# Optimization experiments

Measured on AMD Instinct MI355X. Metric: run time of the kernel, lower is better.

## Reference

```python
import jax, jax.numpy as jnp
import numpy as np

NUM_BINS = 64
R = 2                      # kernel_radius = ceil(2*sigma), sigma=1
NB = NUM_BINS + 2 * R      # 68 padded bins
EPS = 1e-8


def _bspline(d):
    # cubic B-spline Parzen kernel, sigma=1 so d/sigma == d
    ad = jnp.abs(d)
    return jnp.where(
        ad < 1.0, (3.0 * ad ** 3 - 6.0 * ad ** 2 + 4.0) / 6.0,
        jnp.where(ad < 2.0, (2.0 - ad) ** 3 / 6.0, jnp.zeros_like(ad)))


def setup_inputs() -> dict:
    key = jax.random.key(0)
    k1, k2 = jax.random.split(key)
    shape = (2, 1, 80, 80, 80)
    source = jax.random.normal(k1, shape, dtype=jnp.float32)
    target = jax.random.normal(k2, shape, dtype=jnp.float32)
    return {"source": source, "target": target}


def _win(x):
    # x: [B, N] flattened voxels (mask=None, sample_rate=1 keeps all voxels)
    # returns win_idx [B, 2R, N] int32 and bspline weights [B, 2R, N]
    mx = jax.lax.stop_gradient(jnp.max(x, axis=1))            # [B]
    mn = jax.lax.stop_gradient(jnp.min(x, axis=1))            # [B]
    bw = (mx - mn) / NUM_BINS                                 # bin width
    pad_min = mn - bw * R
    pos = (x - pad_min[:, None]) / bw[:, None]                # [B, N]
    idx = jax.lax.stop_gradient(
        jnp.clip(jnp.floor(pos), R, R + NUM_BINS - 1))        # detached floor+clamp
    min_win = (idx - R + 1).astype(jnp.int32)                 # [B, N]
    r = jnp.arange(2 * R, dtype=jnp.int32)                    # [2R]
    win_idx = min_win[:, None, :] + r[None, :, None]          # [B, 2R, N]
    # bin_center is arange(NB), so gathered centers == win_idx as float
    w = _bspline(pos[:, None, :] - win_idx.astype(x.dtype))   # [B, 2R, N]
    return win_idx, w


def _densify(win_idx, w):
    # scatter-add window weights into dense [B, NB, N] bin-weight matrix.
    # (Equivalent to the torch eq-mask-and-sum loop: window indices are distinct.)
    B, _, N = w.shape
    col = jnp.broadcast_to(jnp.arange(N), win_idx.shape[1:])  # [2R, N]
    def per_b(ib, wb):
        return jnp.zeros((NB, N), wb.dtype).at[ib, col].add(wb)
    return jax.vmap(per_b)(win_idx, w)


def reference(source, target):
    B = source.shape[0]
    s = source.reshape(B, -1)   # [B, N]
    t = target.reshape(B, -1)
    si, sw = _win(s)
    ti, tw = _win(t)
    sbw = _densify(si, sw)      # [B, NB, N]
    tbw = _densify(ti, tw)      # [B, NB, N]
    source_hist = sbw.sum(-1)   # [B, NB]
    target_hist = tbw.sum(-1)
    joint_hist = jnp.einsum('bin,bjn->bij', sbw, tbw)   # [B, NB, NB]
    source_density = source_hist / jnp.maximum(source_hist.sum(-1, keepdims=True), EPS)
    target_density = target_hist / jnp.maximum(target_hist.sum(-1, keepdims=True), EPS)
    joint_density = joint_hist / jnp.maximum(joint_hist.sum(axis=(1, 2), keepdims=True), EPS)
    return (source_density, target_density, joint_density)
```

## Files before the change

kernel.cpp:

```cpp
#include <hip/hip_runtime.h>
#include <float.h>

#define NB 68
#define NJ (NB * NB)
#define NSLICE 4
#define HTPB 1024
#define MMBLK 125
#define SCALE 8192.0f


__global__ __launch_bounds__(1024) void k_prep(const float* __restrict__ src,
                                               const float* __restrict__ tgt,
                                               float4* __restrict__ P,
                                               unsigned* __restrict__ J,
                                               int n4) {
    __shared__ float red[16][4];
    const int b = blockIdx.y;
    const int lin = (b * gridDim.x + blockIdx.x) * 1024 + threadIdx.x;
    if (lin < NSLICE * 2 * NJ) J[lin] = 0u;

    const int i = blockIdx.x * 1024 + threadIdx.x;
    float smx = -FLT_MAX, smn = FLT_MAX, tmx = -FLT_MAX, tmn = FLT_MAX;
    if (i < n4) {
        float4 v = ((const float4*)src)[(size_t)b * n4 + i];
        float4 w = ((const float4*)tgt)[(size_t)b * n4 + i];
        smx = fmaxf(fmaxf(v.x, v.y), fmaxf(v.z, v.w));
        smn = fminf(fminf(v.x, v.y), fminf(v.z, v.w));
        tmx = fmaxf(fmaxf(w.x, w.y), fmaxf(w.z, w.w));
        tmn = fminf(fminf(w.x, w.y), fminf(w.z, w.w));
    }
#pragma unroll
    for (int m = 1; m < 64; m <<= 1) {
        smx = fmaxf(smx, __shfl_xor(smx, m));
        smn = fminf(smn, __shfl_xor(smn, m));
        tmx = fmaxf(tmx, __shfl_xor(tmx, m));
        tmn = fminf(tmn, __shfl_xor(tmn, m));
    }
    const int wave = threadIdx.x >> 6;
    if ((threadIdx.x & 63) == 0) {
        red[wave][0] = smx;
        red[wave][1] = smn;
        red[wave][2] = tmx;
        red[wave][3] = tmn;
    }
    __syncthreads();
    if (threadIdx.x == 0) {
#pragma unroll
        for (int k = 1; k < 16; ++k) {
            smx = fmaxf(smx, red[k][0]);
            smn = fminf(smn, red[k][1]);
            tmx = fmaxf(tmx, red[k][2]);
            tmn = fminf(tmn, red[k][3]);
        }
        P[b * 128 + blockIdx.x] = make_float4(smx, smn, tmx, tmn);
    }
}

__device__ __forceinline__ float bspl(float d) {
    float ad = fabsf(d);
    float a = (3.0f * ad * ad * ad - 6.0f * ad * ad + 4.0f) * (1.0f / 6.0f);
    float t = 2.0f - ad;
    float c = t * t * t * (1.0f / 6.0f);
    return ad < 1.0f ? a : (ad < 2.0f ? c : 0.0f);
}

__device__ __forceinline__ void vox1(float sv, float tv, unsigned* jh,
                                     float spad, float sinv, float tpad,
                                     float tinv) {
    float posS = (sv - spad) * sinv;
    float fS = floorf(posS);
    fS = fminf(fmaxf(fS, 2.0f), 65.0f);
    int si = (int)fS - 1;
    float dS = posS - fS;
    float a[4] = {bspl(dS + 1.0f), bspl(dS), bspl(dS - 1.0f), bspl(dS - 2.0f)};

    float posT = (tv - tpad) * tinv;
    float fT = floorf(posT);
    fT = fminf(fmaxf(fT, 2.0f), 65.0f);
    int ti = (int)fT - 1;
    float dT = posT - fT;
    float bb[4] = {bspl(dT + 1.0f), bspl(dT), bspl(dT - 1.0f), bspl(dT - 2.0f)};

    unsigned* base = jh + si * NB + ti;
#pragma unroll
    for (int r = 0; r < 4; ++r) {
#pragma unroll
        for (int c = 0; c < 4; ++c) {
            unsigned q = (unsigned)(a[r] * bb[c] * SCALE + 0.5f);
            atomicAdd(&base[r * NB + c], q);
        }
    }
}

__global__ __launch_bounds__(HTPB) void k_hist(
    const float* __restrict__ src, const float* __restrict__ tgt,
    const float4* __restrict__ P, unsigned* __restrict__ J, int n4) {
    __shared__ unsigned lh[2 * NJ];
    __shared__ float pmm[8], mmv[4];
    const int tid = threadIdx.x;
    const int b = blockIdx.y;

    if (tid < 128) {
        float smx = -FLT_MAX, smn = FLT_MAX, tmx = -FLT_MAX, tmn = FLT_MAX;
        if (tid < MMBLK) {
            float4 v = P[b * 128 + tid];
            smx = v.x; smn = v.y; tmx = v.z; tmn = v.w;
        }
#pragma unroll
        for (int m = 1; m < 64; m <<= 1) {
            smx = fmaxf(smx, __shfl_xor(smx, m));
            smn = fminf(smn, __shfl_xor(smn, m));
            tmx = fmaxf(tmx, __shfl_xor(tmx, m));
            tmn = fminf(tmn, __shfl_xor(tmn, m));
        }
        if ((tid & 63) == 0) {
            int w = tid >> 6;
            pmm[w * 4 + 0] = smx;
            pmm[w * 4 + 1] = smn;
            pmm[w * 4 + 2] = tmx;
            pmm[w * 4 + 3] = tmn;
        }
    }
    uint4* z4 = (uint4*)lh;
    const uint4 zz = make_uint4(0u, 0u, 0u, 0u);
    for (int i = tid; i < (2 * NJ) / 4; i += HTPB) z4[i] = zz;
    __syncthreads();
    if (tid == 0) {
        mmv[0] = fmaxf(pmm[0], pmm[4]);
        mmv[1] = fminf(pmm[1], pmm[5]);
        mmv[2] = fmaxf(pmm[2], pmm[6]);
        mmv[3] = fminf(pmm[3], pmm[7]);
    }
    __syncthreads();

    const float sbw = (mmv[0] - mmv[1]) * (1.0f / 64.0f);
    const float tbw = (mmv[2] - mmv[3]) * (1.0f / 64.0f);
    const float sinv = 1.0f / sbw, tinv = 1.0f / tbw;
    const float spad = mmv[1] - 2.0f * sbw;
    const float tpad = mmv[3] - 2.0f * tbw;

    unsigned* jh = lh + (tid & 1) * NJ;
    const int i0 = blockIdx.x * HTPB + tid;
    if (i0 < n4) {
        float4 sA = ((const float4*)src)[(size_t)b * n4 + i0];
        float4 tA = ((const float4*)tgt)[(size_t)b * n4 + i0];
        vox1(sA.x, tA.x, jh, spad, sinv, tpad, tinv);
        vox1(sA.y, tA.y, jh, spad, sinv, tpad, tinv);
        vox1(sA.z, tA.z, jh, spad, sinv, tpad, tinv);
        vox1(sA.w, tA.w, jh, spad, sinv, tpad, tinv);
    }
    __syncthreads();

    const int rot = (blockIdx.x * 1327) % NJ;
    unsigned* Jb = J + ((size_t)(blockIdx.x & (NSLICE - 1)) * 2 + b) * NJ;
    for (int k = tid; k < NJ; k += HTPB) {
        int i = k + rot;
        if (i >= NJ) i -= NJ;
        unsigned s = lh[i] + lh[NJ + i];
        if (s) atomicAdd(&Jb[i], s);
    }
}

__global__ __launch_bounds__(1024) void k_norm(
    const unsigned* __restrict__ J, float* __restrict__ out, double inv) {
    __shared__ float jf[NJ];
    __shared__ float part[NB][8];
    const int b = blockIdx.x;
    const int tid = threadIdx.x;

    for (int i = tid; i < NJ; i += 1024) {
        unsigned s = 0u;
#pragma unroll
        for (int sl = 0; sl < NSLICE; ++sl)
            s += J[((size_t)sl * 2 + b) * NJ + i];
        float f = (float)((double)s * inv);
        jf[i] = f;
        out[4 * NB + b * NJ + i] = f;
    }
    __syncthreads();

    if (tid < 8 * NB) {
        int r = tid >> 3, k = tid & 7;
        float s = 0.0f;
#pragma unroll
        for (int j = 0; j < 9; ++j) {
            int c = k + 8 * j;
            if (c < NB) s += jf[r * NB + c];
        }
        part[r][k] = s;
    }
    __syncthreads();
    if (tid < NB) {
        float s = part[tid][0] + part[tid][1] + part[tid][2] + part[tid][3] +
                  part[tid][4] + part[tid][5] + part[tid][6] + part[tid][7];
        out[b * NB + tid] = s;
    }
    __syncthreads();

    if (tid < 8 * NB) {
        int c = tid >> 3, k = tid & 7;
        float s = 0.0f;
#pragma unroll
        for (int j = 0; j < 9; ++j) {
            int r = k + 8 * j;
            if (r < NB) s += jf[r * NB + c];
        }
        part[c][k] = s;
    }
    __syncthreads();
    if (tid < NB) {
        float s = part[tid][0] + part[tid][1] + part[tid][2] + part[tid][3] +
                  part[tid][4] + part[tid][5] + part[tid][6] + part[tid][7];
        out[2 * NB + b * NB + tid] = s;
    }
}

extern "C" void kernel_launch(void* const* d_in, const int* in_sizes, int n_in,
                              void* d_out, int out_size, void* d_ws,
                              size_t ws_size, hipStream_t stream) {
    const float* src = (const float*)d_in[0];
    const float* tgt = (const float*)d_in[1];
    float* out = (float*)d_out;
    float4* P = (float4*)((char*)d_ws + 64);
    unsigned* J = (unsigned*)((char*)d_ws + 4160);
    const int nvox = in_sizes[0] / 2;
    const int n4 = nvox / 4;
    const double inv = 1.0 / ((double)nvox * (double)SCALE);

    k_prep<<<dim3(MMBLK, 2), dim3(1024), 0, stream>>>(src, tgt, P, J, n4);
    k_hist<<<dim3(MMBLK, 2), dim3(HTPB), 0, stream>>>(src, tgt, P, J, n4);
    k_norm<<<dim3(2), dim3(1024), 0, stream>>>(J, out, inv);
}
```

Before: 22.15 us.

## Pack histogram atomics into 64-bit pairs with parity-offset LDS copies

Each voxel's 16 shared-memory 32-bit atomic adds become 8 64-bit atomic adds, with two adjacent bin counts packed into one 64-bit word. To keep the 64-bit targets 8-byte aligned, the two LDS histogram copies are now chosen by the parity of the target bin, the second copy offset by one word, instead of by thread parity. The quantization scale doubles to SCALE 16384. This relies on no carry crossing between the packed 32-bit halves, which holds only while per-block counts stay under 2^32. Larger counts at the doubled scale bring that limit closer.

```diff
diff --git a/kernel.cpp b/kernel.cpp
--- a/kernel.cpp
+++ b/kernel.cpp
@@ -6,7 +6,8 @@
 #define NSLICE 4
 #define HTPB 1024
 #define MMBLK 125
-#define SCALE 8192.0f
+#define SCALE 16384.0f
+#define LHSZ (2 * NJ + 8)
 
 
 __global__ __launch_bounds__(1024) void k_prep(const float* __restrict__ src,
@@ -64,7 +65,7 @@
     return ad < 1.0f ? a : (ad < 2.0f ? c : 0.0f);
 }
 
-__device__ __forceinline__ void vox1(float sv, float tv, unsigned* jh,
+__device__ __forceinline__ void vox1(float sv, float tv, unsigned* lh,
                                      float spad, float sinv, float tpad,
                                      float tinv) {
     float posS = (sv - spad) * sinv;
@@ -79,23 +80,27 @@
     fT = fminf(fmaxf(fT, 2.0f), 65.0f);
     int ti = (int)fT - 1;
     float dT = posT - fT;
-    float bb[4] = {bspl(dT + 1.0f), bspl(dT), bspl(dT - 1.0f), bspl(dT - 2.0f)};
-
-    unsigned* base = jh + si * NB + ti;
+    float b0 = bspl(dT + 1.0f), b1 = bspl(dT), b2 = bspl(dT - 1.0f),
+          b3 = bspl(dT - 2.0f);
+
+    unsigned* base = lh + ((ti & 1) ? (NJ + 1) : 0) + si * NB + ti;
 #pragma unroll
     for (int r = 0; r < 4; ++r) {
-#pragma unroll
-        for (int c = 0; c < 4; ++c) {
-            unsigned q = (unsigned)(a[r] * bb[c] * SCALE + 0.5f);
-            atomicAdd(&base[r * NB + c], q);
-        }
+        unsigned q0 = (unsigned)(a[r] * b0 * SCALE + 0.5f);
+        unsigned q1 = (unsigned)(a[r] * b1 * SCALE + 0.5f);
+        unsigned q2 = (unsigned)(a[r] * b2 * SCALE + 0.5f);
+        unsigned q3 = (unsigned)(a[r] * b3 * SCALE + 0.5f);
+        atomicAdd((unsigned long long*)(base + r * NB),
+                  (unsigned long long)q0 | ((unsigned long long)q1 << 32));
+        atomicAdd((unsigned long long*)(base + r * NB + 2),
+                  (unsigned long long)q2 | ((unsigned long long)q3 << 32));
     }
 }
 
 __global__ __launch_bounds__(HTPB) void k_hist(
     const float* __restrict__ src, const float* __restrict__ tgt,
     const float4* __restrict__ P, unsigned* __restrict__ J, int n4) {
-    __shared__ unsigned lh[2 * NJ];
+    __shared__ __align__(16) unsigned lh[LHSZ];
     __shared__ float pmm[8], mmv[4];
     const int tid = threadIdx.x;
     const int b = blockIdx.y;
@@ -123,7 +128,7 @@
     }
     uint4* z4 = (uint4*)lh;
     const uint4 zz = make_uint4(0u, 0u, 0u, 0u);
-    for (int i = tid; i < (2 * NJ) / 4; i += HTPB) z4[i] = zz;
+    for (int i = tid; i < LHSZ / 4; i += HTPB) z4[i] = zz;
     __syncthreads();
     if (tid == 0) {
         mmv[0] = fmaxf(pmm[0], pmm[4]);
@@ -139,15 +144,14 @@
     const float spad = mmv[1] - 2.0f * sbw;
     const float tpad = mmv[3] - 2.0f * tbw;
 
-    unsigned* jh = lh + (tid & 1) * NJ;
     const int i0 = blockIdx.x * HTPB + tid;
     if (i0 < n4) {
         float4 sA = ((const float4*)src)[(size_t)b * n4 + i0];
         float4 tA = ((const float4*)tgt)[(size_t)b * n4 + i0];
-        vox1(sA.x, tA.x, jh, spad, sinv, tpad, tinv);
-        vox1(sA.y, tA.y, jh, spad, sinv, tpad, tinv);
-        vox1(sA.z, tA.z, jh, spad, sinv, tpad, tinv);
-        vox1(sA.w, tA.w, jh, spad, sinv, tpad, tinv);
+        vox1(sA.x, tA.x, lh, spad, sinv, tpad, tinv);
+        vox1(sA.y, tA.y, lh, spad, sinv, tpad, tinv);
+        vox1(sA.z, tA.z, lh, spad, sinv, tpad, tinv);
+        vox1(sA.w, tA.w, lh, spad, sinv, tpad, tinv);
     }
     __syncthreads();
 
@@ -156,7 +160,7 @@
     for (int k = tid; k < NJ; k += HTPB) {
         int i = k + rot;
         if (i >= NJ) i -= NJ;
-        unsigned s = lh[i] + lh[NJ + i];
+        unsigned s = lh[i] + lh[NJ + 1 + i];
         if (s) atomicAdd(&Jb[i], s);
     }
 }
```

Result: no change. 22.22 us (median of 2 runs) (+0.3%).
